# Kernel optimization log

Hardware: AMD Instinct MI355X
Metric: run time of the kernel (lower is better)

The kernel has to match this reference:

```python
import jax, jax.numpy as jnp
import numpy as np

B, C, G = 8, 64, 65536
IN_DIM, OUT_DIM = 64, 64
SLOPE = 0.1


def setup_inputs() -> dict:
    key = jax.random.key(0)
    ks = jax.random.split(key, 5)
    features = jax.random.normal(ks[0], (B, C, G), dtype=jnp.float32)
    # Conv2d(in*2, out, 1, bias=False) weights, squeezed to [out, in*2]
    W0 = jax.random.normal(ks[1], (OUT_DIM, IN_DIM * 2), dtype=jnp.float32) * (1.0 / np.sqrt(IN_DIM * 2))
    W1 = jax.random.normal(ks[2], (OUT_DIM, OUT_DIM * 2), dtype=jnp.float32) * (1.0 / np.sqrt(OUT_DIM * 2))
    W2 = jax.random.normal(ks[3], (OUT_DIM, OUT_DIM * 2), dtype=jnp.float32) * (1.0 / np.sqrt(OUT_DIM * 2))
    W3 = jax.random.normal(ks[4], (OUT_DIM, OUT_DIM * 2), dtype=jnp.float32) * (1.0 / np.sqrt(OUT_DIM * 2))
    return {"features": features, "W0": W0, "W1": W1, "W2": W2, "W3": W3}


def _layer(x, W):
    # x: [B, C, G]; tile the first group's features and build (x, x - x0)
    x0 = x[:, :, :1]                               # [B, C, 1]
    h = jnp.concatenate([x, x - x0], axis=1)       # [B, 2C, G]
    # 1x1 conv == pointwise linear over channels
    y = jnp.einsum("oc,bcg->bog", W, h)            # [B, O, G]
    return jax.nn.leaky_relu(y, negative_slope=SLOPE)


def reference(features, W0, W1, W2, W3):
    x = features
    for W in (W0, W1, W2, W3):
        x = _layer(x, W)
    return jnp.max(x, axis=-1)                     # [B, O]
```

## Files before the change

### kernel.cpp

```cpp
#include <hip/hip_runtime.h>
#include <hip/hip_bf16.h>


#define G_TOT 65536
#define NB 8

typedef _Float16 half4 __attribute__((ext_vector_type(4)));
typedef float float4_ __attribute__((ext_vector_type(4)));


__global__ __launch_bounds__(512) void ge_prep(
    const float* __restrict__ feat,
    const float* __restrict__ W0, const float* __restrict__ W1,
    const float* __restrict__ W2, const float* __restrict__ W3,
    float* __restrict__ ws)
{
    const int tid = threadIdx.x;
    unsigned* maxenc = (unsigned*)(ws + 18432);
    if (tid < 512) maxenc[tid] = 0u;

    for (int i = tid; i < 4 * 64 * 64; i += 512) {
        int l = i >> 12, o = (i >> 6) & 63, c = i & 63;
        const float* Wl = (l == 0) ? W0 : (l == 1) ? W1 : (l == 2) ? W2 : W3;
        ws[i] = Wl[o * 128 + c] + Wl[o * 128 + 64 + c];
    }

    __shared__ float xA[NB][64];
    __shared__ float xB[NB][64];
    {
        int b = tid >> 6, c = tid & 63;
        xA[b][c] = feat[(size_t)(b * 64 + c) * G_TOT];
    }
    __syncthreads();
    float* bias = ws + 16384;
    for (int l = 0; l < 4; ++l) {
        const float* Wl = (l == 0) ? W0 : (l == 1) ? W1 : (l == 2) ? W2 : W3;
        const float* src = (l & 1) ? &xB[0][0] : &xA[0][0];
        float*       dst = (l & 1) ? &xA[0][0] : &xB[0][0];
        int b = tid >> 6, o = tid & 63;
        float s1 = 0.f, s2 = 0.f;
        for (int c = 0; c < 64; ++c) {
            float xv = src[b * 64 + c];
            s1 += Wl[o * 128 + c] * xv;
            s2 += Wl[o * 128 + 64 + c] * xv;
        }
        bias[l * 512 + b * 64 + o] = s2;
        dst[b * 64 + o] = fmaxf(s1, 0.1f * s1);
        __syncthreads();
    }
}

__global__ __launch_bounds__(256, 2) void ge_main(
    const float* __restrict__ feat,
    const float* __restrict__ ws_wa,
    const float* __restrict__ ws_bias,
    unsigned* __restrict__ maxenc)
{
    __shared__ _Float16 lwa[4 * 64 * 68];
    __shared__ float blockmax[4][64];
    const int tid = threadIdx.x;

    for (int i = tid; i < 4 * 64 * 64; i += 256) {
        int l = i >> 12, o = (i >> 6) & 63, c = i & 63;
        lwa[(l * 64 + o) * 68 + c] = (_Float16)ws_wa[i];
    }
    __syncthreads();

    const int w = tid >> 6, lane = tid & 63;
    const int q = lane >> 4, n = lane & 15;
    const int b  = blockIdx.x >> 8;
    const int g0 = ((blockIdx.x & 255) << 8) + (w << 6);

    const float* Xb    = feat + (size_t)b * 64 * G_TOT;
    const float* biasb = ws_bias + b * 64;

    float rmax[4][4];
#pragma unroll
    for (int mt = 0; mt < 4; ++mt)
#pragma unroll
        for (int j = 0; j < 4; ++j) rmax[mt][j] = -__builtin_inff();

#pragma unroll 1
    for (int nt = 0; nt < 4; ++nt) {
        const int gcol = g0 + (nt << 4) + n;

        half4 bf[4];
#pragma unroll
        for (int kf = 0; kf < 4; ++kf) {
            int kbase = (kf << 4) + (q << 2);
            float x0v = Xb[(size_t)(kbase + 0) * G_TOT + gcol];
            float x1v = Xb[(size_t)(kbase + 1) * G_TOT + gcol];
            float x2v = Xb[(size_t)(kbase + 2) * G_TOT + gcol];
            float x3v = Xb[(size_t)(kbase + 3) * G_TOT + gcol];
            half4 t; t[0] = (_Float16)x0v; t[1] = (_Float16)x1v;
            t[2] = (_Float16)x2v; t[3] = (_Float16)x3v;
            bf[kf] = t;
        }

#pragma unroll
        for (int l = 0; l < 4; ++l) {
            float4_ acc[4];
#pragma unroll
            for (int mt = 0; mt < 4; ++mt) { acc[mt][0]=0.f; acc[mt][1]=0.f; acc[mt][2]=0.f; acc[mt][3]=0.f; }
#pragma unroll
            for (int mt = 0; mt < 4; ++mt) {
#pragma unroll
                for (int kf = 0; kf < 4; ++kf) {
                    const _Float16* ap = &lwa[(l * 64 + (mt << 4) + n) * 68 + (kf << 4) + (q << 2)];
                    half4 a = *(const half4*)ap;
                    acc[mt] = __builtin_amdgcn_mfma_f32_16x16x16f16(a, bf[kf], acc[mt], 0, 0, 0);
                }
            }
#pragma unroll
            for (int mt = 0; mt < 4; ++mt) {
                float4_ bb = *(const float4_*)&biasb[l * 512 + (mt << 4) + (q << 2)];
                float y0 = acc[mt][0] - bb[0]; y0 = fmaxf(y0, 0.1f * y0);
                float y1 = acc[mt][1] - bb[1]; y1 = fmaxf(y1, 0.1f * y1);
                float y2 = acc[mt][2] - bb[2]; y2 = fmaxf(y2, 0.1f * y2);
                float y3 = acc[mt][3] - bb[3]; y3 = fmaxf(y3, 0.1f * y3);
                if (l == 3) {
                    rmax[mt][0] = fmaxf(rmax[mt][0], y0);
                    rmax[mt][1] = fmaxf(rmax[mt][1], y1);
                    rmax[mt][2] = fmaxf(rmax[mt][2], y2);
                    rmax[mt][3] = fmaxf(rmax[mt][3], y3);
                } else {
                    half4 t; t[0] = (_Float16)y0; t[1] = (_Float16)y1;
                    t[2] = (_Float16)y2; t[3] = (_Float16)y3;
                    bf[mt] = t;
                }
            }
        }
    }

#pragma unroll
    for (int mt = 0; mt < 4; ++mt)
#pragma unroll
        for (int j = 0; j < 4; ++j) {
            float v = rmax[mt][j];
            v = fmaxf(v, __shfl_xor(v, 1, 64));
            v = fmaxf(v, __shfl_xor(v, 2, 64));
            v = fmaxf(v, __shfl_xor(v, 4, 64));
            v = fmaxf(v, __shfl_xor(v, 8, 64));
            rmax[mt][j] = v;
        }
    if (n == 0) {
#pragma unroll
        for (int mt = 0; mt < 4; ++mt)
#pragma unroll
            for (int j = 0; j < 4; ++j)
                blockmax[w][(mt << 4) + (q << 2) + j] = rmax[mt][j];
    }
    __syncthreads();
    if (tid < 64) {
        float v = fmaxf(fmaxf(blockmax[0][tid], blockmax[1][tid]),
                        fmaxf(blockmax[2][tid], blockmax[3][tid]));
        unsigned s = __float_as_uint(v);
        unsigned enc = (s & 0x80000000u) ? ~s : (s | 0x80000000u);
        atomicMax(&maxenc[b * 64 + tid], enc);
    }
}

__global__ void ge_final(const unsigned* __restrict__ maxenc, float* __restrict__ out)
{
    int i = threadIdx.x;
    if (i < 512) {
        unsigned u = maxenc[i];
        unsigned s = (u & 0x80000000u) ? (u ^ 0x80000000u) : ~u;
        out[i] = __uint_as_float(s);
    }
}

extern "C" void kernel_launch(void* const* d_in, const int* in_sizes, int n_in,
                              void* d_out, int out_size, void* d_ws, size_t ws_size,
                              hipStream_t stream) {
    const float* feat = (const float*)d_in[0];
    const float* W0 = (const float*)d_in[1];
    const float* W1 = (const float*)d_in[2];
    const float* W2 = (const float*)d_in[3];
    const float* W3 = (const float*)d_in[4];
    float* ws = (float*)d_ws;
    unsigned* maxenc = (unsigned*)(ws + 18432);

    ge_prep<<<1, 512, 0, stream>>>(feat, W0, W1, W2, W3, ws);
    ge_main<<<2048, 256, 0, stream>>>(feat, ws, ws + 16384, maxenc);
    ge_final<<<1, 512, 0, stream>>>(maxenc, (float*)d_out);
}
```

Measured before the change: 266.5 us.

## Prefetch next feature tile, pre-swizzle fp16 weights, fold bias into accumulator init

The main kernel now processes 8 column tiles per wave and half as many blocks. It register-prefetches the next tile's 16 feature values while running MFMAs on the current one, so global load latency is hidden. Weights are pre-swizzled in LDS so each lane reads one 16-byte vector per pair of MFMAs. The negated bias is staged in LDS and used as the accumulator's initial value, and leaky-relu between layers is done in packed fp16. It also raises occupancy hints to 4 blocks/SM and caches W in LDS during prep, at the cost of more registers per thread for the prefetch buffers.

```diff
diff --git a/kernel.cpp b/kernel.cpp
--- a/kernel.cpp
+++ b/kernel.cpp
@@ -1,12 +1,16 @@
 #include <hip/hip_runtime.h>
-#include <hip/hip_bf16.h>
 
 
 #define G_TOT 65536
-#define NB 8
-
-typedef _Float16 half4 __attribute__((ext_vector_type(4)));
+
+typedef _Float16 hf2 __attribute__((ext_vector_type(2)));
+typedef _Float16 hf4 __attribute__((ext_vector_type(4)));
+typedef _Float16 hf8 __attribute__((ext_vector_type(8)));
 typedef float float4_ __attribute__((ext_vector_type(4)));
+
+static __device__ __forceinline__ hf2 pkh(float x, float y) {
+    return __builtin_bit_cast(hf2, __builtin_amdgcn_cvt_pkrtz(x, y));
+}
 
 
 __global__ __launch_bounds__(512) void ge_prep(
@@ -17,7 +21,7 @@
 {
     const int tid = threadIdx.x;
     unsigned* maxenc = (unsigned*)(ws + 18432);
-    if (tid < 512) maxenc[tid] = 0u;
+    maxenc[tid] = 0u;
 
     for (int i = tid; i < 4 * 64 * 64; i += 512) {
         int l = i >> 12, o = (i >> 6) & 63, c = i & 63;
@@ -25,54 +29,60 @@
         ws[i] = Wl[o * 128 + c] + Wl[o * 128 + 64 + c];
     }
 
-    __shared__ float xA[NB][64];
-    __shared__ float xB[NB][64];
-    {
-        int b = tid >> 6, c = tid & 63;
-        xA[b][c] = feat[(size_t)(b * 64 + c) * G_TOT];
-    }
-    __syncthreads();
-    float* bias = ws + 16384;
+    __shared__ float lw[64][129];
+    __shared__ float xA[8][64];
+    __shared__ float xB[8][64];
+    const int b = tid >> 6, o = tid & 63;
+    xA[b][o] = feat[(size_t)(b * 64 + o) * G_TOT];
+
+    float* nbias = ws + 16384;
     for (int l = 0; l < 4; ++l) {
         const float* Wl = (l == 0) ? W0 : (l == 1) ? W1 : (l == 2) ? W2 : W3;
+        for (int i = tid; i < 64 * 128; i += 512) lw[i >> 7][i & 127] = Wl[i];
+        __syncthreads();
         const float* src = (l & 1) ? &xB[0][0] : &xA[0][0];
         float*       dst = (l & 1) ? &xA[0][0] : &xB[0][0];
-        int b = tid >> 6, o = tid & 63;
         float s1 = 0.f, s2 = 0.f;
         for (int c = 0; c < 64; ++c) {
             float xv = src[b * 64 + c];
-            s1 += Wl[o * 128 + c] * xv;
-            s2 += Wl[o * 128 + 64 + c] * xv;
-        }
-        bias[l * 512 + b * 64 + o] = s2;
+            s1 += lw[o][c] * xv;
+            s2 += lw[o][64 + c] * xv;
+        }
+        nbias[b * 256 + l * 64 + o] = -s2;
         dst[b * 64 + o] = fmaxf(s1, 0.1f * s1);
         __syncthreads();
     }
 }
 
-__global__ __launch_bounds__(256, 2) void ge_main(
+__global__ __launch_bounds__(256, 4) void ge_main(
     const float* __restrict__ feat,
     const float* __restrict__ ws_wa,
-    const float* __restrict__ ws_bias,
+    const float* __restrict__ nbias,
     unsigned* __restrict__ maxenc)
 {
-    __shared__ _Float16 lwa[4 * 64 * 68];
+    __shared__ _Float16 lws[16384];
+    __shared__ float lbias[256];
     __shared__ float blockmax[4][64];
     const int tid = threadIdx.x;
-
-    for (int i = tid; i < 4 * 64 * 64; i += 256) {
-        int l = i >> 12, o = (i >> 6) & 63, c = i & 63;
-        lwa[(l * 64 + o) * 68 + c] = (_Float16)ws_wa[i];
-    }
+    const int b = blockIdx.x >> 7;
+
+    for (int gi = tid; gi < 4096; gi += 256) {
+        int kf = gi & 3, ln = (gi >> 2) & 63, mt = (gi >> 8) & 3, l = gi >> 10;
+        int o = (mt << 4) + (ln & 15);
+        int c = (kf << 4) + ((ln >> 4) << 2);
+        float4_ wv = *(const float4_*)&ws_wa[((l << 6) + o) * 64 + c];
+        union { hf2 h2[2]; hf4 h4; } u;
+        u.h2[0] = pkh(wv[0], wv[1]);
+        u.h2[1] = pkh(wv[2], wv[3]);
+        *(hf4*)&lws[gi << 2] = u.h4;
+    }
+    lbias[tid] = nbias[(b << 8) + tid];
     __syncthreads();
 
-    const int w = tid >> 6, lane = tid & 63;
-    const int q = lane >> 4, n = lane & 15;
-    const int b  = blockIdx.x >> 8;
-    const int g0 = ((blockIdx.x & 255) << 8) + (w << 6);
-
-    const float* Xb    = feat + (size_t)b * 64 * G_TOT;
-    const float* biasb = ws_bias + b * 64;
+    const int w = tid >> 6, lane = tid & 63, q = lane >> 4, n = lane & 15;
+    const int g0 = ((blockIdx.x & 127) << 9) + (w << 7);
+    const float* Xrow = feat + (size_t)b * 64 * G_TOT + (size_t)(q << 2) * G_TOT;
+    const hf4 k01 = { (_Float16)0.1f, (_Float16)0.1f, (_Float16)0.1f, (_Float16)0.1f };
 
     float rmax[4][4];
 #pragma unroll
@@ -80,55 +90,76 @@
 #pragma unroll
         for (int j = 0; j < 4; ++j) rmax[mt][j] = -__builtin_inff();
 
-#pragma unroll 1
-    for (int nt = 0; nt < 4; ++nt) {
-        const int gcol = g0 + (nt << 4) + n;
-
-        half4 bf[4];
+    float cur[16];
+    {
+        int gcol = g0 + n;
+#pragma unroll
+        for (int kf = 0; kf < 4; ++kf)
+#pragma unroll
+            for (int r = 0; r < 4; ++r)
+                cur[kf * 4 + r] = Xrow[(size_t)((kf << 4) + r) * G_TOT + gcol];
+    }
+
+#pragma unroll 2
+    for (int nt = 0; nt < 8; ++nt) {
+        float nxt[16];
+        if (nt < 7) {
+            int gcol = g0 + ((nt + 1) << 4) + n;
+#pragma unroll
+            for (int kf = 0; kf < 4; ++kf)
+#pragma unroll
+                for (int r = 0; r < 4; ++r)
+                    nxt[kf * 4 + r] = Xrow[(size_t)((kf << 4) + r) * G_TOT + gcol];
+        }
+
+        hf4 bf[4];
 #pragma unroll
         for (int kf = 0; kf < 4; ++kf) {
-            int kbase = (kf << 4) + (q << 2);
-            float x0v = Xb[(size_t)(kbase + 0) * G_TOT + gcol];
-            float x1v = Xb[(size_t)(kbase + 1) * G_TOT + gcol];
-            float x2v = Xb[(size_t)(kbase + 2) * G_TOT + gcol];
-            float x3v = Xb[(size_t)(kbase + 3) * G_TOT + gcol];
-            half4 t; t[0] = (_Float16)x0v; t[1] = (_Float16)x1v;
-            t[2] = (_Float16)x2v; t[3] = (_Float16)x3v;
-            bf[kf] = t;
+            union { hf2 h2[2]; hf4 h4; } u;
+            u.h2[0] = pkh(cur[kf * 4 + 0], cur[kf * 4 + 1]);
+            u.h2[1] = pkh(cur[kf * 4 + 2], cur[kf * 4 + 3]);
+            bf[kf] = u.h4;
         }
 
 #pragma unroll
         for (int l = 0; l < 4; ++l) {
             float4_ acc[4];
 #pragma unroll
-            for (int mt = 0; mt < 4; ++mt) { acc[mt][0]=0.f; acc[mt][1]=0.f; acc[mt][2]=0.f; acc[mt][3]=0.f; }
+            for (int mt = 0; mt < 4; ++mt)
+                acc[mt] = *(const float4_*)&lbias[(l << 6) + (mt << 4) + (q << 2)];
 #pragma unroll
             for (int mt = 0; mt < 4; ++mt) {
 #pragma unroll
-                for (int kf = 0; kf < 4; ++kf) {
-                    const _Float16* ap = &lwa[(l * 64 + (mt << 4) + n) * 68 + (kf << 4) + (q << 2)];
-                    half4 a = *(const half4*)ap;
-                    acc[mt] = __builtin_amdgcn_mfma_f32_16x16x16f16(a, bf[kf], acc[mt], 0, 0, 0);
+                for (int pr = 0; pr < 2; ++pr) {
+                    union { hf8 h8; hf4 h4[2]; } ua;
+                    ua.h8 = *(const hf8*)&lws[(((((l << 2) + mt) << 6) + lane) << 4) + (pr << 3)];
+                    acc[mt] = __builtin_amdgcn_mfma_f32_16x16x16f16(ua.h4[0], bf[(pr << 1) + 0], acc[mt], 0, 0, 0);
+                    acc[mt] = __builtin_amdgcn_mfma_f32_16x16x16f16(ua.h4[1], bf[(pr << 1) + 1], acc[mt], 0, 0, 0);
                 }
             }
-#pragma unroll
-            for (int mt = 0; mt < 4; ++mt) {
-                float4_ bb = *(const float4_*)&biasb[l * 512 + (mt << 4) + (q << 2)];
-                float y0 = acc[mt][0] - bb[0]; y0 = fmaxf(y0, 0.1f * y0);
-                float y1 = acc[mt][1] - bb[1]; y1 = fmaxf(y1, 0.1f * y1);
-                float y2 = acc[mt][2] - bb[2]; y2 = fmaxf(y2, 0.1f * y2);
-                float y3 = acc[mt][3] - bb[3]; y3 = fmaxf(y3, 0.1f * y3);
-                if (l == 3) {
-                    rmax[mt][0] = fmaxf(rmax[mt][0], y0);
-                    rmax[mt][1] = fmaxf(rmax[mt][1], y1);
-                    rmax[mt][2] = fmaxf(rmax[mt][2], y2);
-                    rmax[mt][3] = fmaxf(rmax[mt][3], y3);
-                } else {
-                    half4 t; t[0] = (_Float16)y0; t[1] = (_Float16)y1;
-                    t[2] = (_Float16)y2; t[3] = (_Float16)y3;
-                    bf[mt] = t;
+            if (l < 3) {
+#pragma unroll
+                for (int mt = 0; mt < 4; ++mt) {
+                    union { hf2 h2[2]; hf4 h4; } u;
+                    u.h2[0] = pkh(acc[mt][0], acc[mt][1]);
+                    u.h2[1] = pkh(acc[mt][2], acc[mt][3]);
+                    hf4 h = u.h4;
+                    h = __builtin_elementwise_max(h, h * k01);
+                    bf[mt] = h;
                 }
+            } else {
+#pragma unroll
+                for (int mt = 0; mt < 4; ++mt)
+#pragma unroll
+                    for (int j = 0; j < 4; ++j) {
+                        float y = acc[mt][j];
+                        rmax[mt][j] = fmaxf(rmax[mt][j], fmaxf(y, 0.1f * y));
+                    }
             }
+        }
+        if (nt < 7) {
+#pragma unroll
+            for (int i = 0; i < 16; ++i) cur[i] = nxt[i];
         }
     }
 
@@ -182,6 +213,6 @@
     unsigned* maxenc = (unsigned*)(ws + 18432);
 
     ge_prep<<<1, 512, 0, stream>>>(feat, W0, W1, W2, W3, ws);
-    ge_main<<<2048, 256, 0, stream>>>(feat, ws, ws + 16384, maxenc);
+    ge_main<<<1024, 256, 0, stream>>>(feat, ws, ws + 16384, maxenc);
     ge_final<<<1, 512, 0, stream>>>(maxenc, (float*)d_out);
 }
```

Result: slower. 447.6 us (+67.9%).
